# Optimization experiments

Measured on AMD Instinct MI355X. Metric: run time of the kernel, lower is better.

## Reference

```python
import jax, jax.numpy as jnp
import numpy as np

K = 0.1
GAMMA = 1.0


def setup_inputs() -> dict:
    key = jax.random.key(0)
    k1, k2, k3, k4, k5 = jax.random.split(key, 5)
    N, M, D = 16384, 2048, 128
    # Points must lie inside the Poincare ball (0 < norm < 1) for acos/asin validity.
    x = jax.random.normal(k1, (N, D), dtype=jnp.float32)
    x = x / jnp.linalg.norm(x, axis=1, keepdims=True)
    x = x * jax.random.uniform(k2, (N, 1), minval=0.3, maxval=0.9, dtype=jnp.float32)
    p = jax.random.normal(k3, (M, D), dtype=jnp.float32)
    p = p / jnp.linalg.norm(p, axis=1, keepdims=True)
    p = p * jax.random.uniform(k4, (M, 1), minval=0.3, maxval=0.9, dtype=jnp.float32)
    labels = jax.random.randint(k5, (N,), 0, M)
    return {"x": x, "p": p, "labels": labels}


def reference(x, p, labels):
    N = x.shape[0]
    dot = x @ p.T                                   # [N, M], replaces NxMxD broadcast
    nx2 = jnp.sum(x * x, axis=1, keepdims=True)     # [N, 1] = ||x||^2
    np2 = jnp.sum(p * p, axis=1)                    # [M]    = ||p||^2
    np_norm = jnp.sqrt(np2)                         # [M]

    num = dot * (1.0 + np2) - np2 * (1.0 + nx2)     # [N, M]
    # Faithful to original: sum of squared pairwise distances over the BATCH axis (dim=0)
    # sum_i ||x_i - p_j||^2 = sum_i||x_i||^2 + N*||p_j||^2 - 2*(sum_i x_i)@p_j
    sum_sq_dist = jnp.sum(nx2) + N * np2 - 2.0 * (jnp.sum(x, axis=0) @ p.T)  # [M]
    den = np_norm * jnp.sqrt(sum_sq_dist) * jnp.sqrt(1.0 + np2 * nx2 - 2.0 * dot)  # [N, M]
    angle = jnp.arccos(num / den)                   # [N, M]

    psi = jnp.arcsin(K * (1.0 - np2) / np_norm)     # [M], broadcast over rows
    angles = jnp.maximum(0.0, angle - psi)          # [N, M]

    rows = jnp.arange(N)
    positive = angles[rows, labels]                 # [N]
    neg = jnp.maximum(0.0, GAMMA - angles)          # [N, M]
    negative = jnp.sum(neg, axis=1) - neg[rows, labels]  # exclude label column
    return jnp.mean(positive + negative)
```

## Files before the change

### kernel.cpp

```cpp
#include <hip/hip_runtime.h>
#include <math.h>

#define KCONST 0.1f
#define GAMMA_C 1.0f
#define D_DIM 128

typedef __attribute__((ext_vector_type(8))) short bf16x8;
typedef __attribute__((ext_vector_type(4))) float f32x4;

__device__ __forceinline__ unsigned short f2bf(float f) {
  unsigned int u = __float_as_uint(f);
  u += 0x7fffu + ((u >> 16) & 1u);
  return (unsigned short)(u >> 16);
}

__global__ void prep_x(const float* __restrict__ x, unsigned short* __restrict__ xb,
                       float* __restrict__ nx2p, float* __restrict__ pSumX,
                       float* __restrict__ pS2, int N) {
  const int tid = threadIdx.x;
  const int l = tid & 63, w = tid >> 6;
  const int l16 = l & 15, sub = l >> 4;
  const int waveId = blockIdx.x * 4 + w;
  const float4* x4 = (const float4*)x;
  ushort4* xb4 = (ushort4*)xb;
  float4 c0 = {0.f, 0.f, 0.f, 0.f}, c1 = {0.f, 0.f, 0.f, 0.f};
  float s2 = 0.f;
#pragma unroll
  for (int it = 0; it < 4; ++it) {
    int row = (waveId + it * 1024) * 4 + sub;
    float4 v0 = x4[row * 32 + l16];
    float4 v1 = x4[row * 32 + 16 + l16];
    c0.x += v0.x; c0.y += v0.y; c0.z += v0.z; c0.w += v0.w;
    c1.x += v1.x; c1.y += v1.y; c1.z += v1.z; c1.w += v1.w;
    ushort4 b0, b1;
    b0.x = f2bf(v0.x); b0.y = f2bf(v0.y); b0.z = f2bf(v0.z); b0.w = f2bf(v0.w);
    b1.x = f2bf(v1.x); b1.y = f2bf(v1.y); b1.z = f2bf(v1.z); b1.w = f2bf(v1.w);
    xb4[row * 32 + l16] = b0;
    xb4[row * 32 + 16 + l16] = b1;
    float sq = v0.x * v0.x;
    sq = fmaf(v0.y, v0.y, sq); sq = fmaf(v0.z, v0.z, sq); sq = fmaf(v0.w, v0.w, sq);
    sq = fmaf(v1.x, v1.x, sq); sq = fmaf(v1.y, v1.y, sq);
    sq = fmaf(v1.z, v1.z, sq); sq = fmaf(v1.w, v1.w, sq);
    sq += __shfl_down(sq, 8); sq += __shfl_down(sq, 4);
    sq += __shfl_down(sq, 2); sq += __shfl_down(sq, 1);
    if (l16 == 0) {
      nx2p[row] = 1.f + sq;
      s2 += sq;
    }
  }
  s2 += __shfl_down(s2, 16);
  s2 += __shfl_down(s2, 32);
  __shared__ float cs[128];
  __shared__ float s2w[4];
  if (tid < 128) cs[tid] = 0.f;
  if (l == 0) s2w[w] = s2;
  __syncthreads();
  atomicAdd(&cs[l16 * 4 + 0], c0.x); atomicAdd(&cs[l16 * 4 + 1], c0.y);
  atomicAdd(&cs[l16 * 4 + 2], c0.z); atomicAdd(&cs[l16 * 4 + 3], c0.w);
  atomicAdd(&cs[64 + l16 * 4 + 0], c1.x); atomicAdd(&cs[64 + l16 * 4 + 1], c1.y);
  atomicAdd(&cs[64 + l16 * 4 + 2], c1.z); atomicAdd(&cs[64 + l16 * 4 + 3], c1.w);
  __syncthreads();
  if (tid < 128) pSumX[blockIdx.x * 128 + tid] = cs[tid];
  if (tid == 0) pS2[blockIdx.x] = s2w[0] + s2w[1] + s2w[2] + s2w[3];
}

__global__ void merge_sums(const float* __restrict__ pSumX, const float* __restrict__ pS2,
                           float* __restrict__ sum_x, float* __restrict__ sum_nx2) {
  __shared__ float seg[8][128];
  __shared__ float s2w[4];
  const int t = threadIdx.x;
  const int col = t & 127;
  const int sg = t >> 7;
  float s = 0.f;
#pragma unroll
  for (int b = 0; b < 32; ++b) s += pSumX[(sg * 32 + b) * 128 + col];
  seg[sg][col] = s;
  float s2 = (t < 256) ? pS2[t] : 0.f;
  if (t < 256) {
#pragma unroll
    for (int off = 32; off; off >>= 1) s2 += __shfl_down(s2, off);
    if ((t & 63) == 0) s2w[t >> 6] = s2;
  }
  __syncthreads();
  if (t < 128) {
    float r = 0.f;
#pragma unroll
    for (int k = 0; k < 8; ++k) r += seg[k][col];
    sum_x[t] = r;
  }
  if (t == 0) sum_nx2[0] = s2w[0] + s2w[1] + s2w[2] + s2w[3];
}

__global__ void prep_p(const float* __restrict__ p, unsigned short* __restrict__ pb,
                       const float* __restrict__ sum_x, const float* __restrict__ sum_nx2,
                       float4* __restrict__ colc, float* __restrict__ psiA,
                       int M, int N) {
  const int lane = threadIdx.x & 63;
  const int wave = threadIdx.x >> 6;
  const int j = blockIdx.x * 4 + wave;
  if (j >= M) return;
  const float2* p2 = (const float2*)p;
  ushort2* pb2 = (ushort2*)pb;
  float2 v = p2[j * 64 + lane];
  ushort2 b;
  b.x = f2bf(v.x);
  b.y = f2bf(v.y);
  pb2[j * 64 + lane] = b;
  float np2 = fmaf(v.x, v.x, v.y * v.y);
  float sd = fmaf(v.x, sum_x[2 * lane], v.y * sum_x[2 * lane + 1]);
#pragma unroll
  for (int off = 32; off; off >>= 1) {
    np2 += __shfl_down(np2, off);
    sd += __shfl_down(sd, off);
  }
  if (lane == 0) {
    float ssd = *sum_nx2 + (float)N * np2 - 2.f * sd;
    float npn = sqrtf(np2);
    float cfi = 1.f / (npn * sqrtf(ssd));
    float4 cc;
    cc.x = (1.f + np2) * cfi;
    cc.y = np2 * cfi;
    cc.z = np2;
    cc.w = np2 / (1.f + np2);
    colc[j] = cc;
    psiA[j] = asinf(KCONST * (1.f - np2) / npn);
  }
}

__global__ __launch_bounds__(256, 4) void pair_mfma(
    const unsigned short* __restrict__ xb, const unsigned short* __restrict__ pb,
    const int* __restrict__ labels, const float* __restrict__ nx2p,
    const float4* __restrict__ colc, const float* __restrict__ psiA,
    float* __restrict__ partials) {
  __shared__ float wred[4];
  const int tid = threadIdx.x;
  const int l = tid & 63;
  const int w = tid >> 6;
  const int row0 = blockIdx.y * 128;
  const int col0 = blockIdx.x * 128;
  const int m = tid & 15;
  const int q = (tid >> 4) & 3;
  const int wr = (w & 1) * 64;
  const int wc = (w >> 1) * 64;

  const float4* xg = (const float4*)(xb + (size_t)(row0 + wr) * D_DIM);
  const float4* pg = (const float4*)(pb + (size_t)(col0 + wc) * D_DIM);

  f32x4 acc[4][4];
#pragma unroll
  for (int r = 0; r < 4; ++r)
#pragma unroll
    for (int c = 0; c < 4; ++c) acc[r][c] = (f32x4)(0.f);

#pragma unroll
  for (int s = 0; s < 4; ++s) {
    bf16x8 a[4], b[4];
#pragma unroll
    for (int r = 0; r < 4; ++r)
      a[r] = __builtin_bit_cast(bf16x8, xg[(r * 16 + m) * 16 + s * 4 + q]);
#pragma unroll
    for (int c = 0; c < 4; ++c)
      b[c] = __builtin_bit_cast(bf16x8, pg[(c * 16 + m) * 16 + s * 4 + q]);
#pragma unroll
    for (int r = 0; r < 4; ++r)
#pragma unroll
      for (int c = 0; c < 4; ++c)
        acc[r][c] = __builtin_amdgcn_mfma_f32_16x16x32_bf16(a[r], b[c], acc[r][c], 0, 0, 0);
  }

  float4 cc[4];
  int cols[4];
#pragma unroll
  for (int c = 0; c < 4; ++c) {
    cols[c] = col0 + wc + c * 16 + m;
    cc[c] = colc[cols[c]];
  }
  float4 rnp4v[4];
  int4 lb4v[4];
#pragma unroll
  for (int r = 0; r < 4; ++r) {
    rnp4v[r] = *(const float4*)&nx2p[row0 + wr + r * 16 + q * 4];
    lb4v[r] = *(const int4*)&labels[row0 + wr + r * 16 + q * 4];
  }

  float ssum = 0.f;
#pragma unroll
  for (int r = 0; r < 4; ++r) {
    const f32x4 rnp4 = __builtin_bit_cast(f32x4, rnp4v[r]);
    const int4 lb4 = lb4v[r];
#pragma unroll
    for (int c = 0; c < 4; ++c) {
      const f32x4 dv = acc[r][c];
      const float Tc = cc[c].w;
      float e0 = fmaf(-Tc, rnp4[0], dv[0]);
      float e1 = fmaf(-Tc, rnp4[1], dv[1]);
      float e2 = fmaf(-Tc, rnp4[2], dv[2]);
      float e3 = fmaf(-Tc, rnp4[3], dv[3]);
      float hm = fmaxf(fmaxf(e0, e1), fmaxf(e2, e3));
      bool h = (hm > 0.f) | (cols[c] == lb4.x) | (cols[c] == lb4.y) |
               (cols[c] == lb4.z) | (cols[c] == lb4.w);
      if (__builtin_expect(h, 0)) {
        const float psi = psiA[cols[c]];
        const float C1 = 1.f + psi;
        const float omnp2 = 1.f - cc[c].z;
#pragma unroll
        for (int g = 0; g < 4; ++g) {
          float rnp = rnp4[g];
          float dot = dv[g];
          int lb = (g == 0) ? lb4.x : (g == 1) ? lb4.y : (g == 2) ? lb4.z : lb4.w;
          float den2 = fmaf(cc[c].z, rnp, omnp2) - 2.f * dot;
          float nump = fmaf(dot, cc[c].x, -cc[c].y * rnp);
          float u = nump * __builtin_amdgcn_rsqf(den2);
          u = __builtin_amdgcn_fmed3f(u, -1.f, 1.f);
          float ax = fabsf(u);
          float rt = __builtin_amdgcn_sqrtf(1.f - ax);
          float poly = fmaf(fmaf(fmaf(-0.0187293f, ax, 0.0742610f), ax, -0.2121144f),
                            ax, 1.5707288f);
          float ac = rt * poly;
          ac = (u >= 0.f) ? ac : 3.14159265358979f - ac;
          float neg = __builtin_amdgcn_fmed3f(C1 - ac, 0.f, 1.f);
          float pos = fmaxf(0.f, ac - psi);
          ssum += (cols[c] == lb) ? pos : neg;
        }
      }
    }
  }

#pragma unroll
  for (int off = 32; off; off >>= 1) ssum += __shfl_down(ssum, off);
  if (l == 0) wred[w] = ssum;
  __syncthreads();
  if (tid == 0)
    partials[blockIdx.y * gridDim.x + blockIdx.x] = wred[0] + wred[1] + wred[2] + wred[3];
}

__global__ void finalize(const float* __restrict__ partials, float* __restrict__ out,
                         int n, float invN) {
  float s = 0.f;
  for (int i = threadIdx.x; i < n; i += 256) s += partials[i];
#pragma unroll
  for (int off = 32; off; off >>= 1) s += __shfl_down(s, off);
  __shared__ float wred[4];
  if ((threadIdx.x & 63) == 0) wred[threadIdx.x >> 6] = s;
  __syncthreads();
  if (threadIdx.x == 0) out[0] = (wred[0] + wred[1] + wred[2] + wred[3]) * invN;
}

extern "C" void kernel_launch(void* const* d_in, const int* in_sizes, int n_in,
                              void* d_out, int out_size, void* d_ws, size_t ws_size,
                              hipStream_t stream) {
  const float* x = (const float*)d_in[0];
  const float* p = (const float*)d_in[1];
  const int* labels = (const int*)d_in[2];
  float* out = (float*)d_out;
  const int N = in_sizes[2];
  const int M = in_sizes[1] / D_DIM;

  float* ws = (float*)d_ws;
  float* nx2p = ws;
  float4* colc = (float4*)(ws + N);
  float* psiA = ws + N + 4 * M;
  unsigned short* xb = (unsigned short*)(ws + N + 5 * M);
  unsigned short* pb = (unsigned short*)(ws + N + 5 * M + 64 * N);
  float* pSumX = ws + N + 5 * M + 64 * N + 64 * M;
  float* pS2 = pSumX + 256 * 128;
  float* sum_x = pS2 + 256;
  float* sum_nx2 = sum_x + 128;
  float* partials = sum_nx2 + 4;

  prep_x<<<256, 256, 0, stream>>>(x, xb, nx2p, pSumX, pS2, N);
  merge_sums<<<1, 1024, 0, stream>>>(pSumX, pS2, sum_x, sum_nx2);
  prep_p<<<M / 4, 256, 0, stream>>>(p, pb, sum_x, sum_nx2, colc, psiA, M, N);

  dim3 grid(M / 128, N / 128);
  pair_mfma<<<grid, 256, 0, stream>>>(xb, pb, labels, nx2p, colc, psiA, partials);

  finalize<<<1, 256, 0, stream>>>(partials, out, 2048, 1.0f / (float)N);
}
```

Measured before the change: 113.9 us.

## Stage x tile in LDS via async copy and fuse final reduction with atomics

Loads the block's 128-row bf16 x tile into shared memory using global-to-LDS async copies with an XOR swizzle, so the two waves sharing rows read it from LDS rather than each reading global memory. Removes the separate finalize kernel by having each block atomically add its scaled partial sum into the output, which prep_x zeroes. This adds 32KB of LDS per block and a barrier, and makes the floating-point summation order nondeterministic.

```diff
diff --git a/kernel.cpp b/kernel.cpp
--- a/kernel.cpp
+++ b/kernel.cpp
@@ -7,6 +7,11 @@
 
 typedef __attribute__((ext_vector_type(8))) short bf16x8;
 typedef __attribute__((ext_vector_type(4))) float f32x4;
+
+#define ASYNC_COPY16(gsrc, ldst)                                                  \
+  __builtin_amdgcn_global_load_lds(                                               \
+      (const __attribute__((address_space(1))) void*)(gsrc),                      \
+      (__attribute__((address_space(3))) void*)(ldst), 16, 0, 0)
 
 __device__ __forceinline__ unsigned short f2bf(float f) {
   unsigned int u = __float_as_uint(f);
@@ -16,7 +21,8 @@
 
 __global__ void prep_x(const float* __restrict__ x, unsigned short* __restrict__ xb,
                        float* __restrict__ nx2p, float* __restrict__ pSumX,
-                       float* __restrict__ pS2, int N) {
+                       float* __restrict__ pS2, float* __restrict__ out_zero, int N) {
+  if (blockIdx.x == 0 && threadIdx.x == 0) *out_zero = 0.f;
   const int tid = threadIdx.x;
   const int l = tid & 63, w = tid >> 6;
   const int l16 = l & 15, sub = l >> 4;
@@ -131,19 +137,30 @@
     const unsigned short* __restrict__ xb, const unsigned short* __restrict__ pb,
     const int* __restrict__ labels, const float* __restrict__ nx2p,
     const float4* __restrict__ colc, const float* __restrict__ psiA,
-    float* __restrict__ partials) {
+    float* __restrict__ out, float invN) {
+  __shared__ float4 xs4[2048];
   __shared__ float wred[4];
+
   const int tid = threadIdx.x;
   const int l = tid & 63;
   const int w = tid >> 6;
   const int row0 = blockIdx.y * 128;
   const int col0 = blockIdx.x * 128;
+  const float4* xg = (const float4*)(xb + (size_t)row0 * D_DIM);
+
+#pragma unroll
+  for (int ci = w; ci < 32; ci += 4) {
+    int qi = ci * 64 + l;
+    int r = qi >> 4, ql = qi & 15;
+    int srcq = r * 16 + (ql ^ (r & 15));
+    ASYNC_COPY16(xg + srcq, xs4 + ci * 64);
+  }
+  __syncthreads();
+
   const int m = tid & 15;
   const int q = (tid >> 4) & 3;
   const int wr = (w & 1) * 64;
   const int wc = (w >> 1) * 64;
-
-  const float4* xg = (const float4*)(xb + (size_t)(row0 + wr) * D_DIM);
   const float4* pg = (const float4*)(pb + (size_t)(col0 + wc) * D_DIM);
 
   f32x4 acc[4][4];
@@ -154,13 +171,14 @@
 
 #pragma unroll
   for (int s = 0; s < 4; ++s) {
+    const int qphys = (s * 4 + q) ^ m;
     bf16x8 a[4], b[4];
-#pragma unroll
-    for (int r = 0; r < 4; ++r)
-      a[r] = __builtin_bit_cast(bf16x8, xg[(r * 16 + m) * 16 + s * 4 + q]);
 #pragma unroll
     for (int c = 0; c < 4; ++c)
       b[c] = __builtin_bit_cast(bf16x8, pg[(c * 16 + m) * 16 + s * 4 + q]);
+#pragma unroll
+    for (int r = 0; r < 4; ++r)
+      a[r] = __builtin_bit_cast(bf16x8, xs4[(wr + r * 16 + m) * 16 + qphys]);
 #pragma unroll
     for (int r = 0; r < 4; ++r)
 #pragma unroll
@@ -231,19 +249,7 @@
   if (l == 0) wred[w] = ssum;
   __syncthreads();
   if (tid == 0)
-    partials[blockIdx.y * gridDim.x + blockIdx.x] = wred[0] + wred[1] + wred[2] + wred[3];
-}
-
-__global__ void finalize(const float* __restrict__ partials, float* __restrict__ out,
-                         int n, float invN) {
-  float s = 0.f;
-  for (int i = threadIdx.x; i < n; i += 256) s += partials[i];
-#pragma unroll
-  for (int off = 32; off; off >>= 1) s += __shfl_down(s, off);
-  __shared__ float wred[4];
-  if ((threadIdx.x & 63) == 0) wred[threadIdx.x >> 6] = s;
-  __syncthreads();
-  if (threadIdx.x == 0) out[0] = (wred[0] + wred[1] + wred[2] + wred[3]) * invN;
+    atomicAdd(out, (wred[0] + wred[1] + wred[2] + wred[3]) * invN);
 }
 
 extern "C" void kernel_launch(void* const* d_in, const int* in_sizes, int n_in,
@@ -266,14 +272,12 @@
   float* pS2 = pSumX + 256 * 128;
   float* sum_x = pS2 + 256;
   float* sum_nx2 = sum_x + 128;
-  float* partials = sum_nx2 + 4;
-
-  prep_x<<<256, 256, 0, stream>>>(x, xb, nx2p, pSumX, pS2, N);
+
+  prep_x<<<256, 256, 0, stream>>>(x, xb, nx2p, pSumX, pS2, out, N);
   merge_sums<<<1, 1024, 0, stream>>>(pSumX, pS2, sum_x, sum_nx2);
   prep_p<<<M / 4, 256, 0, stream>>>(p, pb, sum_x, sum_nx2, colc, psiA, M, N);
 
   dim3 grid(M / 128, N / 128);
-  pair_mfma<<<grid, 256, 0, stream>>>(xb, pb, labels, nx2p, colc, psiA, partials);
-
-  finalize<<<1, 256, 0, stream>>>(partials, out, 2048, 1.0f / (float)N);
-}
+  pair_mfma<<<grid, 256, 0, stream>>>(xb, pb, labels, nx2p, colc, psiA, out,
+                                      1.0f / (float)N);
+}
```

Measured after the change: 115.2 us. Within noise of the previous version (+1.2%).

## Stage x tile in LDS and stream double-buffered p tiles via async loads

Applied to the files above, without the earlier changes.

The pair kernel becomes a persistent-style kernel with 512 blocks. Each block loads its 128-row x tile once into LDS through global_load_lds, then loops over 8 column tiles of 64, double-buffering p tiles with async copies and an XOR swizzle to avoid bank conflicts. This removes the repeated global loads of x and p fragments straight into registers across 2048 blocks, and replaces them with LDS reuse and overlapped prefetch. The cost is a __syncthreads each iteration, about 64KB of LDS per block, which lowers occupancy (launch bounds drop from 4 to 2), and fewer blocks overall.

```diff
diff --git a/kernel.cpp b/kernel.cpp
--- a/kernel.cpp
+++ b/kernel.cpp
@@ -7,6 +7,11 @@
 
 typedef __attribute__((ext_vector_type(8))) short bf16x8;
 typedef __attribute__((ext_vector_type(4))) float f32x4;
+
+#define ASYNC_COPY16(gsrc, ldst)                                                  \
+  __builtin_amdgcn_global_load_lds(                                               \
+      (const __attribute__((address_space(1))) void*)(gsrc),                      \
+      (__attribute__((address_space(3))) void*)(ldst), 16, 0, 0)
 
 __device__ __forceinline__ unsigned short f2bf(float f) {
   unsigned int u = __float_as_uint(f);
@@ -127,100 +132,132 @@
   }
 }
 
-__global__ __launch_bounds__(256, 4) void pair_mfma(
+__global__ __launch_bounds__(256, 2) void pair_mfma(
     const unsigned short* __restrict__ xb, const unsigned short* __restrict__ pb,
     const int* __restrict__ labels, const float* __restrict__ nx2p,
     const float4* __restrict__ colc, const float* __restrict__ psiA,
     float* __restrict__ partials) {
+  __shared__ float4 xs4[2048];
+  __shared__ float4 ps4[2][1024];
   __shared__ float wred[4];
+
+  const int b = blockIdx.x;
+  const int rowTile = b >> 2;
+  const int cg = b & 3;
+  const int row0 = rowTile * 128;
+
   const int tid = threadIdx.x;
   const int l = tid & 63;
   const int w = tid >> 6;
-  const int row0 = blockIdx.y * 128;
-  const int col0 = blockIdx.x * 128;
+  const float4* xg = (const float4*)(xb + (size_t)row0 * D_DIM);
+
+#pragma unroll
+  for (int ci = w; ci < 32; ci += 4) {
+    int qi = ci * 64 + l;
+    int r = qi >> 4, ql = qi & 15;
+    ASYNC_COPY16(xg + r * 16 + (ql ^ (r & 15)), xs4 + ci * 64);
+  }
+  {
+    const float4* pg = (const float4*)(pb + (size_t)(cg * 8) * 64 * D_DIM);
+#pragma unroll
+    for (int ci = w; ci < 16; ci += 4) {
+      int qi = ci * 64 + l;
+      int r = qi >> 4, ql = qi & 15;
+      ASYNC_COPY16(pg + r * 16 + (ql ^ (r & 15)), ps4[0] + ci * 64);
+    }
+  }
+
   const int m = tid & 15;
   const int q = (tid >> 4) & 3;
   const int wr = (w & 1) * 64;
-  const int wc = (w >> 1) * 64;
-
-  const float4* xg = (const float4*)(xb + (size_t)(row0 + wr) * D_DIM);
-  const float4* pg = (const float4*)(pb + (size_t)(col0 + wc) * D_DIM);
-
-  f32x4 acc[4][4];
-#pragma unroll
-  for (int r = 0; r < 4; ++r)
-#pragma unroll
-    for (int c = 0; c < 4; ++c) acc[r][c] = (f32x4)(0.f);
-
-#pragma unroll
-  for (int s = 0; s < 4; ++s) {
-    bf16x8 a[4], b[4];
-#pragma unroll
-    for (int r = 0; r < 4; ++r)
-      a[r] = __builtin_bit_cast(bf16x8, xg[(r * 16 + m) * 16 + s * 4 + q]);
-#pragma unroll
-    for (int c = 0; c < 4; ++c)
-      b[c] = __builtin_bit_cast(bf16x8, pg[(c * 16 + m) * 16 + s * 4 + q]);
-#pragma unroll
-    for (int r = 0; r < 4; ++r)
-#pragma unroll
-      for (int c = 0; c < 4; ++c)
-        acc[r][c] = __builtin_amdgcn_mfma_f32_16x16x32_bf16(a[r], b[c], acc[r][c], 0, 0, 0);
-  }
-
-  float4 cc[4];
-  int cols[4];
-#pragma unroll
-  for (int c = 0; c < 4; ++c) {
-    cols[c] = col0 + wc + c * 16 + m;
-    cc[c] = colc[cols[c]];
-  }
-  float4 rnp4v[4];
+  const int wc = (w >> 1) * 32;
+
+  f32x4 rnp4v[4];
   int4 lb4v[4];
 #pragma unroll
   for (int r = 0; r < 4; ++r) {
-    rnp4v[r] = *(const float4*)&nx2p[row0 + wr + r * 16 + q * 4];
+    rnp4v[r] = __builtin_bit_cast(f32x4, *(const float4*)&nx2p[row0 + wr + r * 16 + q * 4]);
     lb4v[r] = *(const int4*)&labels[row0 + wr + r * 16 + q * 4];
   }
 
   float ssum = 0.f;
-#pragma unroll
-  for (int r = 0; r < 4; ++r) {
-    const f32x4 rnp4 = __builtin_bit_cast(f32x4, rnp4v[r]);
-    const int4 lb4 = lb4v[r];
-#pragma unroll
-    for (int c = 0; c < 4; ++c) {
-      const f32x4 dv = acc[r][c];
-      const float Tc = cc[c].w;
-      float e0 = fmaf(-Tc, rnp4[0], dv[0]);
-      float e1 = fmaf(-Tc, rnp4[1], dv[1]);
-      float e2 = fmaf(-Tc, rnp4[2], dv[2]);
-      float e3 = fmaf(-Tc, rnp4[3], dv[3]);
-      float hm = fmaxf(fmaxf(e0, e1), fmaxf(e2, e3));
-      bool h = (hm > 0.f) | (cols[c] == lb4.x) | (cols[c] == lb4.y) |
-               (cols[c] == lb4.z) | (cols[c] == lb4.w);
-      if (__builtin_expect(h, 0)) {
-        const float psi = psiA[cols[c]];
-        const float C1 = 1.f + psi;
-        const float omnp2 = 1.f - cc[c].z;
-#pragma unroll
-        for (int g = 0; g < 4; ++g) {
-          float rnp = rnp4[g];
-          float dot = dv[g];
-          int lb = (g == 0) ? lb4.x : (g == 1) ? lb4.y : (g == 2) ? lb4.z : lb4.w;
-          float den2 = fmaf(cc[c].z, rnp, omnp2) - 2.f * dot;
-          float nump = fmaf(dot, cc[c].x, -cc[c].y * rnp);
-          float u = nump * __builtin_amdgcn_rsqf(den2);
-          u = __builtin_amdgcn_fmed3f(u, -1.f, 1.f);
-          float ax = fabsf(u);
-          float rt = __builtin_amdgcn_sqrtf(1.f - ax);
-          float poly = fmaf(fmaf(fmaf(-0.0187293f, ax, 0.0742610f), ax, -0.2121144f),
-                            ax, 1.5707288f);
-          float ac = rt * poly;
-          ac = (u >= 0.f) ? ac : 3.14159265358979f - ac;
-          float neg = __builtin_amdgcn_fmed3f(C1 - ac, 0.f, 1.f);
-          float pos = fmaxf(0.f, ac - psi);
-          ssum += (cols[c] == lb) ? pos : neg;
+  for (int it = 0; it < 8; ++it) {
+    __syncthreads();
+    const int cur = it & 1;
+    if (it < 7) {
+      const float4* pg = (const float4*)(pb + (size_t)(cg * 8 + it + 1) * 64 * D_DIM);
+#pragma unroll
+      for (int ci = w; ci < 16; ci += 4) {
+        int qi = ci * 64 + l;
+        int r = qi >> 4, ql = qi & 15;
+        ASYNC_COPY16(pg + r * 16 + (ql ^ (r & 15)), ps4[cur ^ 1] + ci * 64);
+      }
+    }
+
+    f32x4 acc[4][2];
+#pragma unroll
+    for (int r = 0; r < 4; ++r) {
+      acc[r][0] = (f32x4)(0.f);
+      acc[r][1] = (f32x4)(0.f);
+    }
+#pragma unroll
+    for (int s = 0; s < 4; ++s) {
+      const int qphys = (s * 4 + q) ^ m;
+      bf16x8 a[4], bf[2];
+#pragma unroll
+      for (int c = 0; c < 2; ++c)
+        bf[c] = __builtin_bit_cast(bf16x8, ps4[cur][(wc + c * 16 + m) * 16 + qphys]);
+#pragma unroll
+      for (int r = 0; r < 4; ++r)
+        a[r] = __builtin_bit_cast(bf16x8, xs4[(wr + r * 16 + m) * 16 + qphys]);
+#pragma unroll
+      for (int r = 0; r < 4; ++r)
+#pragma unroll
+        for (int c = 0; c < 2; ++c)
+          acc[r][c] = __builtin_amdgcn_mfma_f32_16x16x32_bf16(a[r], bf[c], acc[r][c], 0, 0, 0);
+    }
+
+    const int ct0 = (cg * 8 + it) * 64;
+#pragma unroll
+    for (int c = 0; c < 2; ++c) {
+      const int col = ct0 + wc + c * 16 + m;
+      const float4 cc = colc[col];
+      const float Tc = cc.w;
+#pragma unroll
+      for (int r = 0; r < 4; ++r) {
+        const f32x4 rnp4 = rnp4v[r];
+        const int4 lb4 = lb4v[r];
+        const f32x4 dv = acc[r][c];
+        float e0 = fmaf(-Tc, rnp4[0], dv[0]);
+        float e1 = fmaf(-Tc, rnp4[1], dv[1]);
+        float e2 = fmaf(-Tc, rnp4[2], dv[2]);
+        float e3 = fmaf(-Tc, rnp4[3], dv[3]);
+        float hm = fmaxf(fmaxf(e0, e1), fmaxf(e2, e3));
+        bool h = (hm > 0.f) | (col == lb4.x) | (col == lb4.y) |
+                 (col == lb4.z) | (col == lb4.w);
+        if (__builtin_expect(h, 0)) {
+          const float psi = psiA[col];
+          const float C1 = 1.f + psi;
+          const float omnp2 = 1.f - cc.z;
+#pragma unroll
+          for (int g = 0; g < 4; ++g) {
+            float rnp = rnp4[g];
+            float dot = dv[g];
+            int lb = (g == 0) ? lb4.x : (g == 1) ? lb4.y : (g == 2) ? lb4.z : lb4.w;
+            float den2 = fmaf(cc.z, rnp, omnp2) - 2.f * dot;
+            float nump = fmaf(dot, cc.x, -cc.y * rnp);
+            float u = nump * __builtin_amdgcn_rsqf(den2);
+            u = __builtin_amdgcn_fmed3f(u, -1.f, 1.f);
+            float ax = fabsf(u);
+            float rt = __builtin_amdgcn_sqrtf(1.f - ax);
+            float poly = fmaf(fmaf(fmaf(-0.0187293f, ax, 0.0742610f), ax, -0.2121144f),
+                              ax, 1.5707288f);
+            float ac = rt * poly;
+            ac = (u >= 0.f) ? ac : 3.14159265358979f - ac;
+            float neg = __builtin_amdgcn_fmed3f(C1 - ac, 0.f, 1.f);
+            float pos = fmaxf(0.f, ac - psi);
+            ssum += (col == lb) ? pos : neg;
+          }
         }
       }
     }
@@ -231,7 +268,7 @@
   if (l == 0) wred[w] = ssum;
   __syncthreads();
   if (tid == 0)
-    partials[blockIdx.y * gridDim.x + blockIdx.x] = wred[0] + wred[1] + wred[2] + wred[3];
+    partials[b] = wred[0] + wred[1] + wred[2] + wred[3];
 }
 
 __global__ void finalize(const float* __restrict__ partials, float* __restrict__ out,
@@ -272,8 +309,7 @@
   merge_sums<<<1, 1024, 0, stream>>>(pSumX, pS2, sum_x, sum_nx2);
   prep_p<<<M / 4, 256, 0, stream>>>(p, pb, sum_x, sum_nx2, colc, psiA, M, N);
 
-  dim3 grid(M / 128, N / 128);
-  pair_mfma<<<grid, 256, 0, stream>>>(xb, pb, labels, nx2p, colc, psiA, partials);
-
-  finalize<<<1, 256, 0, stream>>>(partials, out, 2048, 1.0f / (float)N);
-}
+  pair_mfma<<<512, 256, 0, stream>>>(xb, pb, labels, nx2p, colc, psiA, partials);
+
+  finalize<<<1, 256, 0, stream>>>(partials, out, 512, 1.0f / (float)N);
+}
```

Result: faster. 94.23 us (-17.3%).
